# Kernel optimization log

Measured on AMD Instinct MI355X. Metric: run time of the kernel, lower is better.

## Reference

```python
import jax, jax.numpy as jnp
import numpy as np

N_NODES = 100000
HIDDEN = 128


def _gcn_conv(x, edge_index, W, b, n_nodes):
    # PyG GCNConv with default symmetric normalization and self-loops.
    src, dst = edge_index[0], edge_index[1]
    loop = jnp.arange(n_nodes, dtype=src.dtype)
    src = jnp.concatenate([src, loop])
    dst = jnp.concatenate([dst, loop])
    # degree over destination nodes (edge weight = 1), self-loops included
    deg = jax.ops.segment_sum(jnp.ones_like(dst, dtype=x.dtype), dst,
                              num_segments=n_nodes)
    dinv = jax.lax.rsqrt(deg)  # deg >= 1 because of self-loops
    norm = dinv[src] * dinv[dst]  # [E+N]
    h = x @ W  # [N, 4H] linear transform first (d_in -> 4H)
    msg = norm[:, None] * h[src]  # [E+N, 4H]
    out = jax.ops.segment_sum(msg, dst, num_segments=n_nodes)
    return out + b


def setup_inputs() -> dict:
    key = jax.random.key(0)
    k1, k2, k3, k4, k5, k6 = jax.random.split(key, 6)
    n, h = N_NODES, HIDDEN
    x = jax.random.normal(k1, (n, h), dtype=jnp.float32)
    h_cur = jax.random.normal(k2, (n, h), dtype=jnp.float32)
    c_cur = jax.random.normal(k3, (n, h), dtype=jnp.float32)
    edge_index = jax.random.randint(k4, (2, 3200000), 0, n, dtype=jnp.int64)
    W = jax.random.normal(k5, (h, 4 * h), dtype=jnp.float32) / np.sqrt(h)
    b = jax.random.normal(k6, (4 * h,), dtype=jnp.float32) * 0.01
    return {"x": x, "edge_index": edge_index, "h_cur": h_cur,
            "c_cur": c_cur, "W": W, "b": b}


def reference(x, edge_index, h_cur, c_cur, W, b):
    combined = x + h_cur  # fused input + hidden add
    conv = _gcn_conv(combined, edge_index, W, b, x.shape[0])  # [N, 4H]
    cc_f = conv[:, :HIDDEN]  # first gate chunk (module returns cc_f only)
    return cc_f
```

## Files before the change

kernel.cpp:

```cpp
#include <hip/hip_runtime.h>
#include <hip/hip_bf16.h>

#define HID 128
#define NGR_SH 7
#define MAXGRP 1024
#define NSB 256
#define CAPH 2560

__device__ __forceinline__ float b2f(unsigned short u) {
    union { unsigned i; float f; } v; v.i = ((unsigned)u) << 16; return v.f;
}
__device__ __forceinline__ unsigned short f2b(float f) {
    unsigned u = __float_as_uint(f);
    return (unsigned short)((u + 0x7fffu + ((u >> 16) & 1u)) >> 16);
}

__global__ __launch_bounds__(256) void histgemm_kernel(const int* __restrict__ ei,
                                                       unsigned* __restrict__ hist,
                                                       const float* __restrict__ x,
                                                       const float* __restrict__ hc,
                                                       const float* __restrict__ W,
                                                       unsigned short* __restrict__ hp,
                                                       int E, int n, int ngroups) {
    __shared__ union {
        unsigned h[MAXGRP];
        float A[64 * 132];
    } sm;
    int tid = threadIdx.x;

    if (blockIdx.x < NSB) {
        for (int g = tid; g < ngroups; g += 256) sm.h[g] = 0u;
        __syncthreads();
        int chunk = (E + NSB - 1) / NSB;
        int beg = blockIdx.x * chunk, end = min(E, beg + chunk);
        for (int i = beg + tid; i < end; i += 256) {
            int dst = ei[(size_t)E + i];
            if ((unsigned)dst < (unsigned)n) atomicAdd(&sm.h[dst >> NGR_SH], 1u);
        }
        __syncthreads();
        for (int g = tid; g < ngroups; g += 256)
            hist[(size_t)blockIdx.x * ngroups + g] = sm.h[g];
    } else {
        int r0 = (blockIdx.x - NSB) * 64;
        for (int i = tid; i < 2048; i += 256) {
            int row = i >> 5;
            int c4 = (i & 31) * 4;
            int grow = r0 + row;
            float4 v;
            if (grow < n) {
                float4 a = *(const float4*)(x + (size_t)grow * HID + c4);
                float4 bb = *(const float4*)(hc + (size_t)grow * HID + c4);
                v = make_float4(a.x + bb.x, a.y + bb.y, a.z + bb.z, a.w + bb.w);
            } else {
                v = make_float4(0.f, 0.f, 0.f, 0.f);
            }
            *(float4*)(&sm.A[row * 132 + c4]) = v;
        }
        __syncthreads();

        int cg = tid & 31;
        int c4 = cg * 4;
        int rg = tid >> 5;
        float acc[8][4];
#pragma unroll
        for (int r = 0; r < 8; ++r) {
            acc[r][0] = 0.f; acc[r][1] = 0.f; acc[r][2] = 0.f; acc[r][3] = 0.f;
        }
#pragma unroll 4
        for (int k = 0; k < 128; ++k) {
            float4 w = *(const float4*)(W + (size_t)k * 512 + c4);
#pragma unroll
            for (int r = 0; r < 8; ++r) {
                float a = sm.A[(rg * 8 + r) * 132 + k];
                acc[r][0] += a * w.x;
                acc[r][1] += a * w.y;
                acc[r][2] += a * w.z;
                acc[r][3] += a * w.w;
            }
        }
#pragma unroll
        for (int r = 0; r < 8; ++r) {
            int grow = r0 + rg * 8 + r;
            if (grow < n) {
                unsigned long long pack =
                    (unsigned long long)f2b(acc[r][0]) |
                    ((unsigned long long)f2b(acc[r][1]) << 16) |
                    ((unsigned long long)f2b(acc[r][2]) << 32) |
                    ((unsigned long long)f2b(acc[r][3]) << 48);
                *(unsigned long long*)(hp + (size_t)grow * HID + c4) = pack;
            }
        }
    }
}

__global__ __launch_bounds__(256) void scan2d_kernel(const unsigned* __restrict__ hist,
                                                     unsigned* __restrict__ base_rel,
                                                     unsigned* __restrict__ gcount,
                                                     int ngroups) {
    int g = blockIdx.x;
    int t = threadIdx.x;
    unsigned v = hist[(size_t)t * ngroups + g];
    int lane = t & 63, w = t >> 6;
    unsigned x = v;
    for (int d = 1; d < 64; d <<= 1) {
        unsigned y = __shfl_up(x, d, 64);
        if (lane >= d) x += y;
    }
    __shared__ unsigned wsum[4];
    if (lane == 63) wsum[w] = x;
    __syncthreads();
    unsigned add = 0;
    for (int ww = 0; ww < 4; ++ww) if (ww < w) add += wsum[ww];
    unsigned incl = x + add;
    base_rel[(size_t)t * ngroups + g] = incl - v;
    if (t == 255) gcount[g] = incl;
}

__global__ __launch_bounds__(1024) void gscan_kernel(const unsigned* __restrict__ gcount,
                                                     unsigned* __restrict__ gboff,
                                                     int ngroups) {
    __shared__ unsigned sums[1024];
    int t = threadIdx.x;
    int chunk = (ngroups + 1023) >> 10;
    int beg = min(t * chunk, ngroups), end = min(beg + chunk, ngroups);
    unsigned local = 0;
    for (int i = beg; i < end; ++i) local += gcount[i];
    sums[t] = local;
    __syncthreads();
    for (int d = 1; d < 1024; d <<= 1) {
        unsigned v = (t >= d) ? sums[t - d] : 0u;
        __syncthreads();
        sums[t] += v;
        __syncthreads();
    }
    unsigned run = (t > 0) ? sums[t - 1] : 0u;
    for (int i = beg; i < end; ++i) { gboff[i] = run; run += gcount[i]; }
    if (t == 1023) gboff[ngroups] = sums[1023];
}

__global__ __launch_bounds__(256) void gscatter_kernel(const int* __restrict__ ei,
                                                       const unsigned* __restrict__ gboff,
                                                       const unsigned* __restrict__ base_rel,
                                                       unsigned* __restrict__ grouped,
                                                       int E, int n, int ngroups) {
    __shared__ unsigned cursor[MAXGRP];
    int blk = blockIdx.x;
    int tid = threadIdx.x;
    for (int g = tid; g < ngroups; g += 256)
        cursor[g] = gboff[g] + base_rel[(size_t)blk * ngroups + g];
    __syncthreads();
    int chunk = (E + NSB - 1) / NSB;
    int beg = blk * chunk, end = min(E, beg + chunk);
    for (int i = beg + tid; i < end; i += 256) {
        int s = ei[i];
        int dst = ei[(size_t)E + i];
        if ((unsigned)dst >= (unsigned)n) continue;
        unsigned ss = (unsigned)min(max(s, 0), n - 1);
        unsigned slot = atomicAdd(&cursor[dst >> NGR_SH], 1u);
        grouped[slot] = ss | ((unsigned)(dst & ((1 << NGR_SH) - 1)) << 17);
    }
}

__global__ __launch_bounds__(256) void dinvg_kernel(const unsigned* __restrict__ grouped,
                                                    const unsigned* __restrict__ gboff,
                                                    float* __restrict__ dinv, int n) {
    __shared__ unsigned lcnt[128];
    int g = blockIdx.x;
    int t = threadIdx.x;
    if (t < 128) lcnt[t] = 0u;
    __syncthreads();
    unsigned s0 = gboff[g], s1 = gboff[g + 1];
    for (unsigned j = s0 + t; j < s1; j += 256) atomicAdd(&lcnt[grouped[j] >> 17], 1u);
    __syncthreads();
    if (t < 128) {
        int node = (g << NGR_SH) + t;
        if (node < n) dinv[node] = rsqrtf((float)(lcnt[t] + 1u));
    }
}

__global__ __launch_bounds__(256) void aggsort_kernel(const unsigned* __restrict__ grouped,
                                                      const unsigned* __restrict__ gboff,
                                                      const float* __restrict__ dinv,
                                                      const unsigned short* __restrict__ hp,
                                                      const float* __restrict__ bias,
                                                      float* __restrict__ out, int n) {
    __shared__ unsigned srcs_lds[CAPH];
    __shared__ unsigned nodeoff[65];
    __shared__ unsigned cursor[64];
    __shared__ float sdinv[64];
    int blk = blockIdx.x;
    unsigned half = blk & 1u;
    int g = blk >> 1;
    int tid = threadIdx.x;
    unsigned s0 = gboff[g], s1 = gboff[g + 1];
    int node0 = (g << NGR_SH) + (int)half * 64;

    if (tid < 64) {
        int node = node0 + tid;
        sdinv[tid] = (node < n) ? dinv[node] : 0.f;
        cursor[tid] = 0u;
    }
    __syncthreads();

    for (unsigned j = s0 + tid; j < s1; j += 256) {
        unsigned p = grouped[j];
        if (((p >> 23) & 1u) == half) atomicAdd(&cursor[(p >> 17) & 63u], 1u);
    }
    __syncthreads();
    if (tid < 64) {
        unsigned v = cursor[tid];
        unsigned x = v;
        for (int d = 1; d < 64; d <<= 1) {
            unsigned y = __shfl_up(x, d, 64);
            if (tid >= d) x += y;
        }
        unsigned excl = x - v;
        nodeoff[tid] = excl;
        cursor[tid] = excl;
        if (tid == 63) nodeoff[64] = x;
    }
    __syncthreads();
    unsigned hcnt = nodeoff[64];

    if (hcnt <= CAPH) {
        for (unsigned j = s0 + tid; j < s1; j += 256) {
            unsigned p = grouped[j];
            if (((p >> 23) & 1u) == half) {
                unsigned slot = atomicAdd(&cursor[(p >> 17) & 63u], 1u);
                srcs_lds[slot] = p & 0x1FFFFu;
            }
        }
        __syncthreads();

        int w = tid >> 6, lane = tid & 63;
        int c = lane * 2;
        for (int nl = w * 16; nl < w * 16 + 16; ++nl) {
            int node = node0 + nl;
            if (node >= n) break;
            unsigned beg = nodeoff[nl], end2 = nodeoff[nl + 1];
            float ax = 0.f, ay = 0.f;
            unsigned i = beg;
            for (; i + 8 <= end2; i += 8) {
                unsigned s[8]; float wd[8]; ushort2 v2[8];
#pragma unroll
                for (int j = 0; j < 8; ++j) s[j] = srcs_lds[i + j];
#pragma unroll
                for (int j = 0; j < 8; ++j) wd[j] = dinv[s[j]];
#pragma unroll
                for (int j = 0; j < 8; ++j) v2[j] = *(const ushort2*)(hp + ((size_t)s[j] << 7) + c);
#pragma unroll
                for (int j = 0; j < 8; ++j) { ax += wd[j] * b2f(v2[j].x); ay += wd[j] * b2f(v2[j].y); }
            }
            if (i < end2) {
                unsigned last = end2 - 1;
                unsigned s[8]; float wd[8]; ushort2 v2[8];
#pragma unroll
                for (int j = 0; j < 8; ++j) {
                    unsigned jj = i + j;
                    s[j] = srcs_lds[jj < end2 ? jj : last];
                    wd[j] = (jj < end2) ? 1.f : 0.f;
                }
#pragma unroll
                for (int j = 0; j < 8; ++j) wd[j] *= dinv[s[j]];
#pragma unroll
                for (int j = 0; j < 8; ++j) v2[j] = *(const ushort2*)(hp + ((size_t)s[j] << 7) + c);
#pragma unroll
                for (int j = 0; j < 8; ++j) { ax += wd[j] * b2f(v2[j].x); ay += wd[j] * b2f(v2[j].y); }
            }
            float dd = sdinv[nl];
            ushort2 hd = *(const ushort2*)(hp + ((size_t)node << 7) + c);
            ax += dd * b2f(hd.x);
            ay += dd * b2f(hd.y);
            float2 bb = *(const float2*)(bias + c);
            float2 res = make_float2(dd * ax + bb.x, dd * ay + bb.y);
            *(float2*)(out + ((size_t)node << 7) + c) = res;
        }
    } else {
        for (int idx = tid; idx < 64 * HID; idx += 256) {
            int ndl = idx >> 7, col = idx & (HID - 1);
            int node = node0 + ndl;
            if (node < n) {
                float dd = sdinv[ndl];
                out[((size_t)node << 7) + col] = dd * dd * b2f(hp[((size_t)node << 7) + col]) + bias[col];
            }
        }
        __syncthreads();
        if (tid < 64) {
            int c = tid * 2;
            for (unsigned j = s0; j < s1; ++j) {
                unsigned p = grouped[j];
                if (((p >> 23) & 1u) != half) continue;
                unsigned dl = (p >> 17) & 63u, s = p & 0x1FFFFu;
                int node = node0 + (int)dl;
                if (node >= n) continue;
                float wsc = dinv[s] * sdinv[dl];
                ushort2 v = *(const ushort2*)(hp + ((size_t)s << 7) + c);
                float2* o = (float2*)(out + ((size_t)node << 7) + c);
                float2 cur = *o;
                cur.x += wsc * b2f(v.x);
                cur.y += wsc * b2f(v.y);
                *o = cur;
            }
        }
    }
}

extern "C" void kernel_launch(void* const* d_in, const int* in_sizes, int n_in,
                              void* d_out, int out_size, void* d_ws, size_t ws_size,
                              hipStream_t stream) {
    const float* x = (const float*)d_in[0];
    const int* ei = (const int*)d_in[1];
    const float* hc = (const float*)d_in[2];
    const float* W = (const float*)d_in[4];
    const float* b = (const float*)d_in[5];
    float* out = (float*)d_out;

    int n = in_sizes[0] / HID;
    int E = in_sizes[1] / 2;
    int ngroups = (n + 127) >> NGR_SH;

    char* ws = (char*)d_ws;
    unsigned* gcount = (unsigned*)(ws);
    unsigned* gboff  = (unsigned*)(ws + 8192);
    float*    dinv   = (float*)   (ws + 16384);
    unsigned* grouped= (unsigned*)(ws + 416384);
    unsigned short* hp = (unsigned short*)(ws + 13216384);

    unsigned* hist     = (unsigned*)d_out;
    unsigned* base_rel = hist + (size_t)NSB * ngroups;

    int gemm_blocks = (n + 63) / 64;
    histgemm_kernel<<<NSB + gemm_blocks, 256, 0, stream>>>(ei, hist, x, hc, W, hp, E, n, ngroups);
    scan2d_kernel<<<ngroups, 256, 0, stream>>>(hist, base_rel, gcount, ngroups);
    gscan_kernel<<<1, 1024, 0, stream>>>(gcount, gboff, ngroups);
    gscatter_kernel<<<NSB, 256, 0, stream>>>(ei, gboff, base_rel, grouped, E, n, ngroups);
    dinvg_kernel<<<ngroups, 256, 0, stream>>>(grouped, gboff, dinv, n);
    aggsort_kernel<<<ngroups * 2, 256, 0, stream>>>(grouped, gboff, dinv, hp, b, out, n);
}
```

Baseline: 252.0 us.

## Bucket edges by source-range tile to improve gather locality in aggregation

Edges within each 64-node half-group are now counted and scattered by a (destination node, source tile) key, with eight tiles of 16K source nodes each, using a 512-entry block-wide scan. The gather loop iterates over source tiles on the outside and over the 16 nodes per wavefront on the inside, keeping 16 register accumulators, so that concurrent blocks touch nearby rows of hp and reuse cache. In exchange it adds more LDS atomics and scan work, uses more registers, and switches to short 4-wide masked batches with more loop overhead per tiny segment.

```diff
diff --git a/kernel.cpp b/kernel.cpp
--- a/kernel.cpp
+++ b/kernel.cpp
@@ -6,6 +6,7 @@
 #define MAXGRP 1024
 #define NSB 256
 #define CAPH 2560
+#define NT 8
 
 __device__ __forceinline__ float b2f(unsigned short u) {
     union { unsigned i; float f; } v; v.i = ((unsigned)u) << 16; return v.f;
@@ -185,9 +186,10 @@
                                                       const float* __restrict__ bias,
                                                       float* __restrict__ out, int n) {
     __shared__ unsigned srcs_lds[CAPH];
-    __shared__ unsigned nodeoff[65];
-    __shared__ unsigned cursor[64];
+    __shared__ unsigned kbase[513];
+    __shared__ unsigned cursor[512];
     __shared__ float sdinv[64];
+    __shared__ unsigned wsum[4];
     int blk = blockIdx.x;
     unsigned half = blk & 1u;
     int g = blk >> 1;
@@ -198,79 +200,102 @@
     if (tid < 64) {
         int node = node0 + tid;
         sdinv[tid] = (node < n) ? dinv[node] : 0.f;
-        cursor[tid] = 0u;
-    }
+    }
+    cursor[tid] = 0u;
+    cursor[tid + 256] = 0u;
     __syncthreads();
 
     for (unsigned j = s0 + tid; j < s1; j += 256) {
         unsigned p = grouped[j];
-        if (((p >> 23) & 1u) == half) atomicAdd(&cursor[(p >> 17) & 63u], 1u);
-    }
-    __syncthreads();
-    if (tid < 64) {
-        unsigned v = cursor[tid];
-        unsigned x = v;
+        if (((p >> 23) & 1u) == half) {
+            unsigned nl = (p >> 17) & 63u;
+            unsigned src = p & 0x1FFFFu;
+            unsigned tt = min(src >> 14, 7u);
+            atomicAdd(&cursor[(nl << 3) | tt], 1u);
+        }
+    }
+    __syncthreads();
+
+    {
+        unsigned c0 = cursor[2 * tid], c1 = cursor[2 * tid + 1];
+        unsigned pair = c0 + c1;
+        int lane = tid & 63, w = tid >> 6;
+        unsigned x = pair;
         for (int d = 1; d < 64; d <<= 1) {
             unsigned y = __shfl_up(x, d, 64);
-            if (tid >= d) x += y;
-        }
-        unsigned excl = x - v;
-        nodeoff[tid] = excl;
-        cursor[tid] = excl;
-        if (tid == 63) nodeoff[64] = x;
-    }
-    __syncthreads();
-    unsigned hcnt = nodeoff[64];
+            if (lane >= d) x += y;
+        }
+        if (lane == 63) wsum[w] = x;
+        __syncthreads();
+        unsigned add = 0;
+        for (int ww = 0; ww < 4; ++ww) if (ww < w) add += wsum[ww];
+        unsigned incl = x + add;
+        unsigned excl = incl - pair;
+        kbase[2 * tid] = excl;
+        kbase[2 * tid + 1] = excl + c0;
+        cursor[2 * tid] = excl;
+        cursor[2 * tid + 1] = excl + c0;
+        if (tid == 255) kbase[512] = incl;
+    }
+    __syncthreads();
+    unsigned hcnt = kbase[512];
 
     if (hcnt <= CAPH) {
         for (unsigned j = s0 + tid; j < s1; j += 256) {
             unsigned p = grouped[j];
             if (((p >> 23) & 1u) == half) {
-                unsigned slot = atomicAdd(&cursor[(p >> 17) & 63u], 1u);
-                srcs_lds[slot] = p & 0x1FFFFu;
+                unsigned nl = (p >> 17) & 63u;
+                unsigned src = p & 0x1FFFFu;
+                unsigned tt = min(src >> 14, 7u);
+                unsigned slot = atomicAdd(&cursor[(nl << 3) | tt], 1u);
+                srcs_lds[slot] = src;
             }
         }
         __syncthreads();
 
         int w = tid >> 6, lane = tid & 63;
         int c = lane * 2;
-        for (int nl = w * 16; nl < w * 16 + 16; ++nl) {
+        float accx[16], accy[16];
+#pragma unroll
+        for (int k = 0; k < 16; ++k) { accx[k] = 0.f; accy[k] = 0.f; }
+
+        for (int t = 0; t < NT; ++t) {
+#pragma unroll
+            for (int k = 0; k < 16; ++k) {
+                int nl = w * 16 + k;
+                unsigned key = ((unsigned)nl << 3) | (unsigned)t;
+                unsigned i0 = kbase[key], i1 = kbase[key + 1];
+                for (unsigned i = i0; i < i1; i += 4) {
+                    unsigned last = i1 - 1;
+                    unsigned s[4]; float wd[4]; ushort2 v2[4];
+#pragma unroll
+                    for (int j = 0; j < 4; ++j) {
+                        unsigned jj = i + j;
+                        s[j] = srcs_lds[jj < i1 ? jj : last];
+                        wd[j] = (jj < i1) ? 1.f : 0.f;
+                    }
+#pragma unroll
+                    for (int j = 0; j < 4; ++j) wd[j] *= dinv[s[j]];
+#pragma unroll
+                    for (int j = 0; j < 4; ++j) v2[j] = *(const ushort2*)(hp + ((size_t)s[j] << 7) + c);
+#pragma unroll
+                    for (int j = 0; j < 4; ++j) {
+                        accx[k] += wd[j] * b2f(v2[j].x);
+                        accy[k] += wd[j] * b2f(v2[j].y);
+                    }
+                }
+            }
+        }
+
+#pragma unroll
+        for (int k = 0; k < 16; ++k) {
+            int nl = w * 16 + k;
             int node = node0 + nl;
-            if (node >= n) break;
-            unsigned beg = nodeoff[nl], end2 = nodeoff[nl + 1];
-            float ax = 0.f, ay = 0.f;
-            unsigned i = beg;
-            for (; i + 8 <= end2; i += 8) {
-                unsigned s[8]; float wd[8]; ushort2 v2[8];
-#pragma unroll
-                for (int j = 0; j < 8; ++j) s[j] = srcs_lds[i + j];
-#pragma unroll
-                for (int j = 0; j < 8; ++j) wd[j] = dinv[s[j]];
-#pragma unroll
-                for (int j = 0; j < 8; ++j) v2[j] = *(const ushort2*)(hp + ((size_t)s[j] << 7) + c);
-#pragma unroll
-                for (int j = 0; j < 8; ++j) { ax += wd[j] * b2f(v2[j].x); ay += wd[j] * b2f(v2[j].y); }
-            }
-            if (i < end2) {
-                unsigned last = end2 - 1;
-                unsigned s[8]; float wd[8]; ushort2 v2[8];
-#pragma unroll
-                for (int j = 0; j < 8; ++j) {
-                    unsigned jj = i + j;
-                    s[j] = srcs_lds[jj < end2 ? jj : last];
-                    wd[j] = (jj < end2) ? 1.f : 0.f;
-                }
-#pragma unroll
-                for (int j = 0; j < 8; ++j) wd[j] *= dinv[s[j]];
-#pragma unroll
-                for (int j = 0; j < 8; ++j) v2[j] = *(const ushort2*)(hp + ((size_t)s[j] << 7) + c);
-#pragma unroll
-                for (int j = 0; j < 8; ++j) { ax += wd[j] * b2f(v2[j].x); ay += wd[j] * b2f(v2[j].y); }
-            }
+            if (node >= n) continue;
             float dd = sdinv[nl];
             ushort2 hd = *(const ushort2*)(hp + ((size_t)node << 7) + c);
-            ax += dd * b2f(hd.x);
-            ay += dd * b2f(hd.y);
+            float ax = accx[k] + dd * b2f(hd.x);
+            float ay = accy[k] + dd * b2f(hd.y);
             float2 bb = *(const float2*)(bias + c);
             float2 res = make_float2(dd * ax + bb.x, dd * ay + bb.y);
             *(float2*)(out + ((size_t)node << 7) + c) = res;
```

Result: slower. 327.2 us (+29.8%).
